# Kernel tuning notes

Measured on AMD Instinct MI355X. Metric: run time of the kernel, lower is better.

Reference implementation:

```python
import jax, jax.numpy as jnp
import numpy as np

B, L, E = 4, 1024, 1024
H, D = 16, 64          # num_heads, head_dim
HID = H * D            # hidden_dim == 1024
R = 4                  # nrels


def setup_inputs() -> dict:
    key = jax.random.key(0)
    ks = jax.random.split(key, 8)
    query = jax.random.normal(ks[0], (B, L, E), dtype=jnp.float32)
    rels = jax.random.uniform(ks[1], (B, L, L, R), dtype=jnp.float32)
    attn_mask = jax.random.normal(ks[2], (B, L, L), dtype=jnp.float32)
    key_padding_mask = jax.random.bernoulli(ks[3], 0.9, (B, L, L))
    # xavier-ish init for linear weights
    proj_w = jax.random.normal(ks[4], (4 * HID, E), dtype=jnp.float32) * (2.0 / (4 * HID + E)) ** 0.5
    proj_b = jnp.zeros((4 * HID,), dtype=jnp.float32)
    out_w = jax.random.normal(ks[5], (E, HID), dtype=jnp.float32) * (2.0 / (E + HID)) ** 0.5
    out_b = jnp.zeros((E,), dtype=jnp.float32)
    rels_bias = jax.random.uniform(ks[6], (R, H), dtype=jnp.float32, minval=-0.1, maxval=0.1)
    return {"query": query, "rels": rels, "attn_mask": attn_mask,
            "key_padding_mask": key_padding_mask, "proj_w": proj_w, "proj_b": proj_b,
            "out_w": out_w, "out_b": out_b, "rels_bias": rels_bias}


def reference(query, rels, attn_mask, key_padding_mask, proj_w, proj_b, out_w, out_b, rels_bias):
    b, l, _ = query.shape
    # fused QKVG projection
    qkvg = query @ proj_w.T + proj_b                       # [b, l, 4*HID]
    q, k, v, g = jnp.split(qkvg, 4, axis=-1)
    q = q.reshape(b, l, H, D)
    k = k.reshape(b, l, H, D)
    v = v.reshape(b, l, H, D)
    g = g.reshape(b, l, H, D)
    scores = jnp.einsum('bihd,bjhd->bijh', q, k)
    scores = scores + jnp.einsum('bijr,rh->bijh', rels, rels_bias)
    scores = scores * (D ** -0.5)
    # NOTE: log_softmax over the HEADS axis (dim=-1), as in the source,
    # then additive log-domain mask over keys, then exp.
    w = jnp.exp(jax.nn.log_softmax(scores, axis=-1) + attn_mask[:, :, :, None])
    w = jnp.where(key_padding_mask[:, :, :, None], w, 0.0)
    attn_out = jnp.einsum('bijh,bjhd->bihd', w, jnp.tanh(v))
    gated = attn_out * jax.nn.sigmoid(g)                   # [b, l, H, D]
    out = gated.reshape(b, l, HID) @ out_w.T + out_b       # [b, l, E]
    return (out, w)
```

## Files before the change

kernel.cpp:

```cpp
#include <hip/hip_runtime.h>

typedef unsigned short u16;
using bf16x8 = __attribute__((ext_vector_type(8))) short;
using f32x4  = __attribute__((ext_vector_type(4))) float;

__device__ __forceinline__ u16 f2bf(float f) {
  unsigned u = __builtin_bit_cast(unsigned, f);
  u += 0x7fffu + ((u >> 16) & 1u);
  return (u16)(u >> 16);
}
__device__ __forceinline__ float bf2f(u16 h) {
  unsigned u = ((unsigned)h) << 16;
  return __builtin_bit_cast(float, u);
}
__device__ __forceinline__ float fast_rcp(float x){ return __builtin_amdgcn_rcpf(x); }
__device__ __forceinline__ float tanh_fast(float x){
  float ax = fabsf(x);
  float e = __expf(-2.f*ax);
  float t = (1.f - e) * fast_rcp(1.f + e);
  return copysignf(t, x);
}
__device__ __forceinline__ float sigmoid_fast(float x){
  return fast_rcp(1.f + __expf(-x));
}

__global__ __launch_bounds__(256) void cvt_bf16(const float* __restrict__ src,
                                                u16* __restrict__ dst, int n){
  int i = (blockIdx.x * 256 + threadIdx.x) * 8;
  if (i >= n) return;
  float4 a = *(const float4*)(src + i);
  float4 b = *(const float4*)(src + i + 4);
  uint4 u;
  u.x = (unsigned)f2bf(a.x) | ((unsigned)f2bf(a.y) << 16);
  u.y = (unsigned)f2bf(a.z) | ((unsigned)f2bf(a.w) << 16);
  u.z = (unsigned)f2bf(b.x) | ((unsigned)f2bf(b.y) << 16);
  u.w = (unsigned)f2bf(b.z) | ((unsigned)f2bf(b.w) << 16);
  *(uint4*)(dst + i) = u;
}

template<int EPI>
__global__ __launch_bounds__(256, 2) void gemm_bt(
    const u16* __restrict__ A, const u16* __restrict__ B, const float* __restrict__ bias,
    u16* __restrict__ oq, u16* __restrict__ ok, u16* __restrict__ ov, u16* __restrict__ og,
    float* __restrict__ outp, int K)
{
  __shared__ u16 a_lds[4*128*8];
  __shared__ u16 b_lds[4*128*8];
  const int tid  = threadIdx.x;
  const int lane = tid & 63;
  const int wv   = tid >> 6;
  const int wr   = wv >> 1, wc = wv & 1;
  const int col  = lane & 15, quad = lane >> 4;
  const int m0   = blockIdx.y * 128, n0 = blockIdx.x * 128;
  f32x4 acc[4][4] = {};
  for (int k0 = 0; k0 < K; k0 += 32) {
    __syncthreads();
    #pragma unroll
    for (int s = 0; s < 2; s++) {
      int cid = tid + 256*s;
      int row = cid >> 2, qk = cid & 3;
      *(bf16x8*)(&a_lds[(qk*128+row)*8]) = *(const bf16x8*)(A + (m0+row)*K + k0 + qk*8);
      *(bf16x8*)(&b_lds[(qk*128+row)*8]) = *(const bf16x8*)(B + (n0+row)*K + k0 + qk*8);
    }
    __syncthreads();
    bf16x8 af[4], bfr[4];
    #pragma unroll
    for (int mi=0;mi<4;mi++) af[mi]  = *(const bf16x8*)(&a_lds[(quad*128 + wr*64 + mi*16 + col)*8]);
    #pragma unroll
    for (int ni=0;ni<4;ni++) bfr[ni] = *(const bf16x8*)(&b_lds[(quad*128 + wc*64 + ni*16 + col)*8]);
    #pragma unroll
    for (int mi=0;mi<4;mi++)
      #pragma unroll
      for (int ni=0;ni<4;ni++)
        acc[mi][ni] = __builtin_amdgcn_mfma_f32_16x16x32_bf16(af[mi], bfr[ni], acc[mi][ni], 0, 0, 0);
  }
  #pragma unroll
  for (int mi=0;mi<4;mi++) {
    #pragma unroll
    for (int ni=0;ni<4;ni++) {
      #pragma unroll
      for (int r=0;r<4;r++) {
        const int m = m0 + wr*64 + mi*16 + quad*4 + r;
        const int n = n0 + wc*64 + ni*16 + col;
        const float val = acc[mi][ni][r] + bias[n];
        if (EPI == 0) {
          const int idx = m*1024 + (n & 1023);
          const int quarter = n0 >> 10;
          if (quarter == 0)      oq[idx] = f2bf(val);
          else if (quarter == 1) ok[idx] = f2bf(val);
          else if (quarter == 2) ov[idx] = f2bf(tanh_fast(val));
          else                   og[idx] = f2bf(sigmoid_fast(val));
        } else {
          outp[m*1024 + n] = val;
        }
      }
    }
  }
}

__global__ __launch_bounds__(256) void vtrans(const u16* __restrict__ vin, u16* __restrict__ vout){
  __shared__ u16 tile[64][68];
  const int bh = blockIdx.y;
  const int b = bh >> 4, h = bh & 15;
  const int i0 = blockIdx.x * 64;
  const int t = threadIdx.x;
  #pragma unroll
  for (int s=0;s<4;s++){
    int idx = t + 256*s;
    int ti = idx >> 4;
    int d4 = (idx & 15) * 4;
    uint2 v = *(const uint2*)(vin + ((size_t)((b*1024 + i0 + ti)*16 + h))*64 + d4);
    tile[ti][d4+0] = (u16)(v.x);
    tile[ti][d4+1] = (u16)(v.x >> 16);
    tile[ti][d4+2] = (u16)(v.y);
    tile[ti][d4+3] = (u16)(v.y >> 16);
  }
  __syncthreads();
  #pragma unroll
  for (int s=0;s<4;s++){
    int idx = t + 256*s;
    int d  = idx >> 4;
    int t4 = (idx & 15) * 4;
    uint2 o;
    o.x = (unsigned)tile[t4+0][d] | ((unsigned)tile[t4+1][d] << 16);
    o.y = (unsigned)tile[t4+2][d] | ((unsigned)tile[t4+3][d] << 16);
    *(uint2*)(vout + ((size_t)((b*16 + h)*64 + d))*1024 + i0 + t4) = o;
  }
}

__global__ __launch_bounds__(256) void attn_kernel(
    const u16* __restrict__ qb, const u16* __restrict__ kb,
    const u16* __restrict__ vt, const u16* __restrict__ sgb,
    const float* __restrict__ rels, const float* __restrict__ amask,
    const int* __restrict__ kpm, const float* __restrict__ rbias,
    float* __restrict__ wout, u16* __restrict__ gated)
{
  __shared__ u16 w_lds[16*16*72];
  const int bid = blockIdx.x;
  const int b  = (bid >> 1) & 3;
  const int it = (bid & 1) | ((bid >> 3) << 1);
  const int i0 = it << 4;
  const int tid = threadIdx.x;
  const int lane = tid & 63;
  const int wv  = tid >> 6;
  const int col = lane & 15, quad = lane >> 4;

  float rbv[4][16];
  #pragma unroll
  for (int r=0;r<4;r++)
    #pragma unroll
    for (int h=0;h<16;h++)
      rbv[r][h] = rbias[r*16+h];

  f32x4 Oa[4][4] = {};

  for (int t = 0; t < 16; t++) {
    const int j0b = t << 6;
    const int j0  = j0b + (wv << 4);
    f32x4 sc[16] = {};
    #pragma unroll
    for (int h=0; h<16; h++) {
      #pragma unroll
      for (int c=0; c<2; c++) {
        bf16x8 aq = *(const bf16x8*)(qb + (size_t)(b*1024 + i0 + col)*1024 + h*64 + c*32 + quad*8);
        bf16x8 bk = *(const bf16x8*)(kb + (size_t)(b*1024 + j0 + col)*1024 + h*64 + c*32 + quad*8);
        sc[h] = __builtin_amdgcn_mfma_f32_16x16x32_bf16(aq, bk, sc[h], 0, 0, 0);
      }
    }
    #pragma unroll
    for (int r=0; r<4; r++) {
      const int i = i0 + quad*4 + r;
      const int j = j0 + col;
      const int pij = (b*1024 + i)*1024 + j;
      const float4 rl = *(const float4*)(rels + (size_t)pij*4);
      const float mk = amask[pij];
      const int   pd = kpm[pij];
      float p[16];
      float mx = -1e30f;
      #pragma unroll
      for (int h=0;h<16;h++) {
        float s = sc[h][r];
        s = fmaf(rl.x, rbv[0][h], s);
        s = fmaf(rl.y, rbv[1][h], s);
        s = fmaf(rl.z, rbv[2][h], s);
        s = fmaf(rl.w, rbv[3][h], s);
        s *= 0.125f;
        p[h] = s;
        mx = fmaxf(mx, s);
      }
      float S = 0.f;
      #pragma unroll
      for (int h=0;h<16;h++) { p[h] = __expf(p[h] - mx); S += p[h]; }
      const float scl = pd ? (__expf(mk) * fast_rcp(S)) : 0.f;
      #pragma unroll
      for (int h=0;h<16;h++) p[h] *= scl;
      float4* wp = (float4*)(wout + (size_t)pij*16);
      wp[0] = make_float4(p[0], p[1], p[2], p[3]);
      wp[1] = make_float4(p[4], p[5], p[6], p[7]);
      wp[2] = make_float4(p[8], p[9], p[10], p[11]);
      wp[3] = make_float4(p[12],p[13],p[14],p[15]);
      #pragma unroll
      for (int h=0;h<16;h++)
        w_lds[(h*16 + quad*4 + r)*72 + (wv<<4) + col] = f2bf(p[h]);
    }
    __syncthreads();
    #pragma unroll
    for (int hh=0; hh<4; hh++) {
      const int h = (wv<<2) + hh;
      #pragma unroll
      for (int c2=0; c2<2; c2++) {
        bf16x8 aw = *(const bf16x8*)(&w_lds[(h*16 + col)*72 + c2*32 + quad*8]);
        #pragma unroll
        for (int dt=0; dt<4; dt++) {
          bf16x8 bv = *(const bf16x8*)(vt + (size_t)((b*16 + h)*64 + dt*16 + col)*1024 + j0b + c2*32 + quad*8);
          Oa[hh][dt] = __builtin_amdgcn_mfma_f32_16x16x32_bf16(aw, bv, Oa[hh][dt], 0, 0, 0);
        }
      }
    }
    __syncthreads();
  }
  #pragma unroll
  for (int hh=0; hh<4; hh++) {
    const int h = (wv<<2) + hh;
    #pragma unroll
    for (int dt=0; dt<4; dt++) {
      #pragma unroll
      for (int r=0; r<4; r++) {
        const int i = i0 + quad*4 + r;
        const int d = dt*16 + col;
        const int idx = ((b*1024 + i)*16 + h)*64 + d;
        const float val = Oa[hh][dt][r] * bf2f(sgb[idx]);
        gated[idx] = f2bf(val);
      }
    }
  }
}

extern "C" void kernel_launch(void* const* d_in, const int* in_sizes, int n_in,
                              void* d_out, int out_size, void* d_ws, size_t ws_size,
                              hipStream_t stream) {
  const float* query  = (const float*)d_in[0];
  const float* rels   = (const float*)d_in[1];
  const float* amask  = (const float*)d_in[2];
  const int*   kpm    = (const int*)d_in[3];
  const float* proj_w = (const float*)d_in[4];
  const float* proj_b = (const float*)d_in[5];
  const float* out_w  = (const float*)d_in[6];
  const float* out_b  = (const float*)d_in[7];
  const float* rbias  = (const float*)d_in[8];

  float* out  = (float*)d_out;
  float* wout = out + (size_t)4*1024*1024;

  char* ws = (char*)d_ws;
  u16* q_b   = (u16*)(ws + ((size_t) 0 << 20));
  u16* k_b   = (u16*)(ws + ((size_t) 8 << 20));
  u16* sg_b  = (u16*)(ws + ((size_t)16 << 20));
  u16* vth   = (u16*)(ws + ((size_t)24 << 20));
  u16* vt    = (u16*)(ws + ((size_t)32 << 20));
  u16* qryb  = (u16*)(ws + ((size_t)40 << 20));
  u16* gated = qryb;
  u16* pwb   = (u16*)(ws + ((size_t)48 << 20));
  u16* owb   = (u16*)(ws + ((size_t)56 << 20));

  cvt_bf16<<<2048, 256, 0, stream>>>(query,  qryb, 4*1024*1024);
  cvt_bf16<<<2048, 256, 0, stream>>>(proj_w, pwb,  4*1024*1024);
  cvt_bf16<<< 512, 256, 0, stream>>>(out_w,  owb,  1024*1024);

  gemm_bt<0><<<dim3(32,32), 256, 0, stream>>>(qryb, pwb, proj_b,
                                              q_b, k_b, vth, sg_b, nullptr, 1024);
  vtrans<<<dim3(16,64), 256, 0, stream>>>(vth, vt);
  attn_kernel<<<256, 256, 0, stream>>>(q_b, k_b, vt, sg_b,
                                       rels, amask, kpm, rbias, wout, gated);
  gemm_bt<1><<<dim3(8,32), 256, 0, stream>>>(gated, owb, out_b,
                                             nullptr, nullptr, nullptr, nullptr, out, 1024);
}
```

Before: 785.5 us.

## Split attention key loop across three blocks with fp16 partials and reduce-gate kernel

The attention kernel now takes a second grid dimension that splits the 16 key tiles into three chunks (6/5/5), giving 768 blocks instead of 256 to fill more of the GPU's compute units. Each chunk writes fp16 partial outputs into reused workspace buffers. A new reduce_gate kernel sums the three partials and applies the sigmoid gate before the output GEMM. Launch bounds ask for 3 blocks per CU. The cost is an extra kernel launch, extra memory traffic for the partials, and fp16 rounding of the partial sums.

```diff
diff --git a/kernel.cpp b/kernel.cpp
--- a/kernel.cpp
+++ b/kernel.cpp
@@ -12,6 +12,9 @@
 __device__ __forceinline__ float bf2f(u16 h) {
   unsigned u = ((unsigned)h) << 16;
   return __builtin_bit_cast(float, u);
+}
+__device__ __forceinline__ float f16f(unsigned bits) {
+  return (float)__builtin_bit_cast(_Float16, (unsigned short)(bits & 0xffffu));
 }
 __device__ __forceinline__ float fast_rcp(float x){ return __builtin_amdgcn_rcpf(x); }
 __device__ __forceinline__ float tanh_fast(float x){
@@ -128,18 +131,22 @@
   }
 }
 
-__global__ __launch_bounds__(256) void attn_kernel(
+__global__ __launch_bounds__(256, 3) void attn_kernel(
     const u16* __restrict__ qb, const u16* __restrict__ kb,
-    const u16* __restrict__ vt, const u16* __restrict__ sgb,
+    const u16* __restrict__ vt,
     const float* __restrict__ rels, const float* __restrict__ amask,
     const int* __restrict__ kpm, const float* __restrict__ rbias,
-    float* __restrict__ wout, u16* __restrict__ gated)
+    float* __restrict__ wout,
+    u16* __restrict__ o0, u16* __restrict__ o1, u16* __restrict__ o2)
 {
   __shared__ u16 w_lds[16*16*72];
   const int bid = blockIdx.x;
   const int b  = (bid >> 1) & 3;
   const int it = (bid & 1) | ((bid >> 3) << 1);
   const int i0 = it << 4;
+  const int js = blockIdx.y;
+  const int t0 = js*5 + (js > 0);
+  const int t1 = t0 + (js == 0 ? 6 : 5);
   const int tid = threadIdx.x;
   const int lane = tid & 63;
   const int wv  = tid >> 6;
@@ -154,7 +161,7 @@
 
   f32x4 Oa[4][4] = {};
 
-  for (int t = 0; t < 16; t++) {
+  for (int t = t0; t < t1; t++) {
     const int j0b = t << 6;
     const int j0  = j0b + (wv << 4);
     f32x4 sc[16] = {};
@@ -219,6 +226,7 @@
     }
     __syncthreads();
   }
+  u16* op = (js == 0) ? o0 : ((js == 1) ? o1 : o2);
   #pragma unroll
   for (int hh=0; hh<4; hh++) {
     const int h = (wv<<2) + hh;
@@ -229,11 +237,37 @@
         const int i = i0 + quad*4 + r;
         const int d = dt*16 + col;
         const int idx = ((b*1024 + i)*16 + h)*64 + d;
-        const float val = Oa[hh][dt][r] * bf2f(sgb[idx]);
-        gated[idx] = f2bf(val);
-      }
-    }
-  }
+        _Float16 hv = (_Float16)Oa[hh][dt][r];
+        op[idx] = __builtin_bit_cast(unsigned short, hv);
+      }
+    }
+  }
+}
+
+__global__ __launch_bounds__(256) void reduce_gate(
+    const u16* o0, const u16* __restrict__ o1, const u16* __restrict__ o2,
+    const u16* __restrict__ sg, u16* gated)
+{
+  const int i = (blockIdx.x * 256 + threadIdx.x) * 8;
+  uint4 a = *(const uint4*)(o0 + i);
+  uint4 b = *(const uint4*)(o1 + i);
+  uint4 c = *(const uint4*)(o2 + i);
+  uint4 s = *(const uint4*)(sg + i);
+  const unsigned* ap = (const unsigned*)&a;
+  const unsigned* bp = (const unsigned*)&b;
+  const unsigned* cp = (const unsigned*)&c;
+  const unsigned* sp = (const unsigned*)&s;
+  uint4 r;
+  unsigned* rp = (unsigned*)&r;
+  #pragma unroll
+  for (int k=0;k<4;k++){
+    float f0 = f16f(ap[k]) + f16f(bp[k]) + f16f(cp[k]);
+    float f1 = f16f(ap[k]>>16) + f16f(bp[k]>>16) + f16f(cp[k]>>16);
+    f0 *= bf2f((u16)(sp[k] & 0xffffu));
+    f1 *= bf2f((u16)(sp[k] >> 16));
+    rp[k] = (unsigned)f2bf(f0) | ((unsigned)f2bf(f1) << 16);
+  }
+  *(uint4*)(gated + i) = r;
 }
 
 extern "C" void kernel_launch(void* const* d_in, const int* in_sizes, int n_in,
@@ -259,9 +293,12 @@
   u16* vth   = (u16*)(ws + ((size_t)24 << 20));
   u16* vt    = (u16*)(ws + ((size_t)32 << 20));
   u16* qryb  = (u16*)(ws + ((size_t)40 << 20));
-  u16* gated = qryb;
   u16* pwb   = (u16*)(ws + ((size_t)48 << 20));
   u16* owb   = (u16*)(ws + ((size_t)56 << 20));
+  u16* o0 = qryb;
+  u16* o1 = pwb;
+  u16* o2 = vth;
+  u16* gated = o0;
 
   cvt_bf16<<<2048, 256, 0, stream>>>(query,  qryb, 4*1024*1024);
   cvt_bf16<<<2048, 256, 0, stream>>>(proj_w, pwb,  4*1024*1024);
@@ -270,8 +307,10 @@
   gemm_bt<0><<<dim3(32,32), 256, 0, stream>>>(qryb, pwb, proj_b,
                                               q_b, k_b, vth, sg_b, nullptr, 1024);
   vtrans<<<dim3(16,64), 256, 0, stream>>>(vth, vt);
-  attn_kernel<<<256, 256, 0, stream>>>(q_b, k_b, vt, sg_b,
-                                       rels, amask, kpm, rbias, wout, gated);
+  attn_kernel<<<dim3(256,3), 256, 0, stream>>>(q_b, k_b, vt,
+                                               rels, amask, kpm, rbias, wout,
+                                               o0, o1, o2);
+  reduce_gate<<<2048, 256, 0, stream>>>(o0, o1, o2, sg_b, gated);
   gemm_bt<1><<<dim3(8,32), 256, 0, stream>>>(gated, owb, out_b,
                                              nullptr, nullptr, nullptr, nullptr, out, 1024);
 }
```

Measured after the change: 759.3 us. 3.3% less time.
